# Optimization experiments

Hardware: AMD Instinct MI355X
Metric: run time of the kernel (lower is better)

## Reference

```python
import jax, jax.numpy as jnp
import numpy as np

B, S, D, NH, NKV, HD, FF = 2, 2048, 2048, 16, 8, 128, 8192
EPS = 1e-6
ROPE_THETA = 10000.0


def rmsnorm(x, w):
    return x * jax.lax.rsqrt(jnp.mean(x * x, axis=-1, keepdims=True) + EPS) * w


def rotate_half(x):
    h = x.shape[-1] // 2
    return jnp.concatenate([-x[..., h:], x[..., :h]], axis=-1)


def setup_inputs() -> dict:
    key = jax.random.key(0)
    ks = jax.random.split(key, 32)
    sc = 0.02
    inp = {}
    inp['x'] = jax.random.normal(ks[0], (B, S, D), dtype=jnp.float32)
    pos = jnp.arange(S, dtype=jnp.float32)
    inv = 1.0 / (ROPE_THETA ** (jnp.arange(0, HD, 2, dtype=jnp.float32) / HD))
    fr = jnp.outer(pos, inv)
    emb = jnp.concatenate([fr, fr], axis=-1)  # [S, HD]
    inp['cos'] = jnp.broadcast_to(jnp.cos(emb)[None], (B, S, HD)).astype(jnp.float32)
    inp['sin'] = jnp.broadcast_to(jnp.sin(emb)[None], (B, S, HD)).astype(jnp.float32)
    inp['vision_token_mask'] = jax.random.randint(ks[1], (B, S), 0, 2) > 0
    inp['attn_norm_w'] = jnp.ones((D,), jnp.float32)
    inp['ffn_norm_w'] = jnp.ones((D,), jnp.float32)
    shapes = {
        'wq': (D, NH * HD), 'wk': (D, NKV * HD), 'wv': (D, NKV * HD), 'wo': (NH * HD, D),
        'mm_wq': (D, NH * HD), 'mm_wk': (D, NKV * HD), 'mm_wv': (D, NKV * HD), 'mm_wo': (NH * HD, D),
        'gate_w': (D, FF), 'up_w': (D, FF), 'down_w': (FF, D),
        'mm_gate_w': (D, FF), 'mm_up_w': (D, FF), 'mm_down_w': (FF, D),
    }
    for i, (name, shp) in enumerate(shapes.items()):
        inp[name] = jax.random.normal(ks[2 + i], shp, dtype=jnp.float32) * sc
    for name in ['q_norm_w', 'k_norm_w', 'mm_q_norm_w', 'mm_k_norm_w']:
        inp[name] = jnp.ones((HD,), jnp.float32)
    return inp


def gpt_block(x, cos, sin, mask, attn_norm_w, ffn_norm_w,
              wq, wk, wv, wo, mm_wq, mm_wk, mm_wv, mm_wo,
              q_norm_w, k_norm_w, mm_q_norm_w, mm_k_norm_w,
              gate_w, up_w, down_w, mm_gate_w, mm_up_w, mm_down_w):
    m2 = mask[..., None]            # [B,S,1]
    m4 = mask[:, :, None, None]     # [B,S,1,1]
    h = rmsnorm(x, attn_norm_w)
    # dual-path QKV: text tokens use plain weights, vision tokens use mm_* weights
    q_t = rmsnorm((h @ wq).reshape(B, S, NH, HD), q_norm_w)
    q_v = rmsnorm((h @ mm_wq).reshape(B, S, NH, HD), mm_q_norm_w)
    q = jnp.where(m4, q_v, q_t)
    k_t = rmsnorm((h @ wk).reshape(B, S, NKV, HD), k_norm_w)
    k_v = rmsnorm((h @ mm_wk).reshape(B, S, NKV, HD), mm_k_norm_w)
    k = jnp.where(m4, k_v, k_t)
    v = jnp.where(m2, h @ mm_wv, h @ wv).reshape(B, S, NKV, HD)
    # RoPE (unsqueeze over head dim)
    cu = cos[:, :, None, :]
    su = sin[:, :, None, :]
    q = q * cu + rotate_half(q) * su
    k = k * cu + rotate_half(k) * su
    # GQA repeat + causal attention
    rep = NH // NKV
    k_r = jnp.repeat(k, rep, axis=2)
    v_r = jnp.repeat(v, rep, axis=2)
    scale = 1.0 / jnp.sqrt(jnp.float32(HD))
    scores = jnp.einsum('bqhd,bkhd->bhqk', q, k_r) * scale
    causal = jnp.tril(jnp.ones((S, S), bool))
    scores = jnp.where(causal, scores, jnp.float32(-1e30))
    p = jax.nn.softmax(scores, axis=-1)
    attn = jnp.einsum('bhqk,bkhd->bqhd', p, v_r).reshape(B, S, NH * HD)
    attn_out = jnp.where(m2, attn @ mm_wo, attn @ wo)
    h2 = x + attn_out
    # dual-path SwiGLU FFN
    g = rmsnorm(h2, ffn_norm_w)
    ff_t = (jax.nn.silu(g @ gate_w) * (g @ up_w)) @ down_w
    ff_v = (jax.nn.silu(g @ mm_gate_w) * (g @ mm_up_w)) @ mm_down_w
    return h2 + jnp.where(m2, ff_v, ff_t)


def reference(x, cos, sin, vision_token_mask, attn_norm_w, ffn_norm_w,
              wq, wk, wv, wo, mm_wq, mm_wk, mm_wv, mm_wo,
              q_norm_w, k_norm_w, mm_q_norm_w, mm_k_norm_w,
              gate_w, up_w, down_w, mm_gate_w, mm_up_w, mm_down_w):
    return gpt_block(x, cos, sin, vision_token_mask, attn_norm_w, ffn_norm_w,
                     wq, wk, wv, wo, mm_wq, mm_wk, mm_wv, mm_wo,
                     q_norm_w, k_norm_w, mm_q_norm_w, mm_k_norm_w,
                     gate_w, up_w, down_w, mm_gate_w, mm_up_w, mm_down_w)
```

## Files before the change

kernel.cpp:

```cpp
#include <hip/hip_runtime.h>

typedef unsigned short u16;
typedef __bf16 bf16x8 __attribute__((ext_vector_type(8)));
typedef float f32x4 __attribute__((ext_vector_type(4)));

__device__ __forceinline__ u16 f2bf(float f) {
    unsigned u = __builtin_bit_cast(unsigned, f);
    u += 0x7fffu + ((u >> 16) & 1u);
    return (u16)(u >> 16);
}
__device__ __forceinline__ float bf2f(u16 v) {
    unsigned u = ((unsigned)v) << 16;
    return __builtin_bit_cast(float, u);
}
__device__ __forceinline__ void glds16(const void* g, void* l) {
    __builtin_amdgcn_global_load_lds(
        (const __attribute__((address_space(1))) unsigned*)g,
        (__attribute__((address_space(3))) unsigned*)l, 16, 0, 0);
}

__device__ __forceinline__ void xcd_map(int bid, int nloc, int& tm, int& tn)
{
    const int TM = 33;
    const int xcd = bid & 7;
    int l = bid >> 3;
    const int per = nloc << 3;
    const int fullC = TM >> 3;
    const int lFull = fullC * per;
    int c, tn_l, tmIn;
    if (l < lFull) { c = l / per; int r = l - c * per; tn_l = r >> 3; tmIn = r & 7; }
    else { int r = l - lFull; int sc = TM - (fullC << 3); c = fullC; tn_l = r / sc; tmIn = r % sc; }
    tm = (c << 3) + tmIn;
    tn = xcd * nloc + tn_l;
}

__global__ __launch_bounds__(1024) void build_perm(
    const int* __restrict__ mask, int* __restrict__ perm, int* __restrict__ counts)
{
    __shared__ int sc[1024];
    int t = threadIdx.x;
    int m[4], cnt = 0;
#pragma unroll
    for (int j = 0; j < 4; j++) {
        m[j] = mask[t * 4 + j] != 0;
        cnt += (m[j] == 0);
    }
    sc[t] = cnt;
    __syncthreads();
    for (int off = 1; off < 1024; off <<= 1) {
        int v = (t >= off) ? sc[t - off] : 0;
        __syncthreads();
        sc[t] += v;
        __syncthreads();
    }
    int totT = sc[1023];
    int exT = sc[t] - cnt;
    int exV = t * 4 - exT;
    int pT = exT, pV = totT + exV;
#pragma unroll
    for (int j = 0; j < 4; j++) {
        if (m[j] == 0) perm[pT++] = t * 4 + j;
        else           perm[pV++] = t * 4 + j;
    }
    if (t == 0) { counts[0] = totT; counts[1] = 4096 - totT; }
}

__global__ __launch_bounds__(256) void transpose_bf16(
    const float* __restrict__ W, u16* __restrict__ Wt, int Kd, int Nd)
{
    __shared__ float tile[32][33];
    int k0 = blockIdx.x * 32, n0 = blockIdx.y * 32;
    int tx = threadIdx.x, ty = threadIdx.y;
#pragma unroll
    for (int i = 0; i < 32; i += 8)
        tile[ty + i][tx] = W[(long)(k0 + ty + i) * Nd + n0 + tx];
    __syncthreads();
#pragma unroll
    for (int i = 0; i < 32; i += 8)
        Wt[(long)(n0 + ty + i) * Kd + k0 + tx] = f2bf(tile[tx][ty + i]);
}

__global__ __launch_bounds__(256) void rms_x(
    const float* __restrict__ x, const float* __restrict__ w, u16* __restrict__ out)
{
    long row = blockIdx.x;
    int t = threadIdx.x, wave = t >> 6, lane = t & 63;
    const float4* x4 = (const float4*)(x + row * 2048);
    float4 a = x4[2 * t], b = x4[2 * t + 1];
    float ss = a.x*a.x + a.y*a.y + a.z*a.z + a.w*a.w
             + b.x*b.x + b.y*b.y + b.z*b.z + b.w*b.w;
#pragma unroll
    for (int m = 1; m < 64; m <<= 1) ss += __shfl_xor(ss, m);
    __shared__ float red[4];
    if (lane == 0) red[wave] = ss;
    __syncthreads();
    float tot = red[0] + red[1] + red[2] + red[3];
    float inv = rsqrtf(tot * (1.0f / 2048.0f) + 1e-6f);
    const float4* w4 = (const float4*)w;
    float4 wa = w4[2 * t], wb = w4[2 * t + 1];
    u16* op = out + row * 2048 + t * 8;
    op[0] = f2bf(a.x * inv * wa.x); op[1] = f2bf(a.y * inv * wa.y);
    op[2] = f2bf(a.z * inv * wa.z); op[3] = f2bf(a.w * inv * wa.w);
    op[4] = f2bf(b.x * inv * wb.x); op[5] = f2bf(b.y * inv * wb.y);
    op[6] = f2bf(b.z * inv * wb.z); op[7] = f2bf(b.w * inv * wb.w);
}

template <int EPI, bool PG, bool PC>
__global__ __launch_bounds__(512, 2) void gemmk(
    const u16* __restrict__ A, const u16* __restrict__ Bt0, const u16* __restrict__ Bt1,
    void* __restrict__ Cv, const float* __restrict__ resid,
    const int* __restrict__ perm, const int* __restrict__ counts, int N, int K)
{
    extern __shared__ u16 lds[];
    int tm, tn;
    xcd_map(blockIdx.x, N >> 11, tm, tn);
    const int nT = counts[0];
    const int tT = (nT + 127) >> 7, tV = (4096 - nT + 127) >> 7;
    if (tm >= tT + tV) return;
    const bool vis = tm >= tT;
    const u16* Bt = vis ? Bt1 : Bt0;
    const int rowbase = vis ? nT + (tm - tT) * 128 : tm * 128;
    const int rowlim = vis ? 4096 : nT;
    const int tid = threadIdx.x;
    const int wave = tid >> 6, lane = tid & 63;
    const int wrbase = (wave >> 2) * 64, wcbase = (wave & 3) * 64;
    const int lr = lane & 15, lg = lane >> 4;
    const int n0 = tn * 256;
    const int t8 = tid >> 3, sp = tid & 7;
    const char* aSrc[2];
    const char* bSrc[4];
#pragma unroll
    for (int c = 0; c < 2; c++) {
        int r = c * 64 + t8;
        int gr = rowbase + r; gr = gr < 4095 ? gr : 4095;
        long ar = PG ? perm[gr] : gr;
        aSrc[c] = (const char*)A + ar * (long)K * 2 + ((sp ^ (r & 7)) << 4);
    }
#pragma unroll
    for (int c = 0; c < 4; c++) {
        int r = c * 64 + t8;
        bSrc[c] = (const char*)Bt + (long)(n0 + r) * K * 2 + ((sp ^ (r & 7)) << 4);
    }
    auto stage = [&](int kt, int bu) {
        char* ab = (char*)lds + bu * 49152;
        char* bb = ab + 16384;
        long ko = (long)kt * 128;
#pragma unroll
        for (int c = 0; c < 2; c++)
            glds16(aSrc[c] + ko, ab + c * 8192 + tid * 16);
#pragma unroll
        for (int c = 0; c < 4; c++)
            glds16(bSrc[c] + ko, bb + c * 8192 + tid * 16);
    };
    auto ldA = [&](int bu, int mi, int kk) -> bf16x8 {
        const char* ab = (const char*)lds + bu * 49152;
        int row = wrbase + mi * 16 + lr;
        int sl = kk * 4 + lg;
        return *(const bf16x8*)(ab + row * 128 + ((sl ^ (row & 7)) << 4));
    };
    auto ldB = [&](int bu, int ni, int kk) -> bf16x8 {
        const char* bb = (const char*)lds + bu * 49152 + 16384;
        int row = wcbase + ni * 16 + lr;
        int sl = kk * 4 + lg;
        return *(const bf16x8*)(bb + row * 128 + ((sl ^ (row & 7)) << 4));
    };

    f32x4 acc[4][4] = {};
    const int nkt = K >> 6;
    stage(0, 0);
    stage(1, 1);
    for (int kt = 0; kt < nkt; ++kt) {
        const int bu = kt % 3;
        if (kt == nkt - 1) asm volatile("s_waitcnt vmcnt(0)" ::: "memory");
        else               asm volatile("s_waitcnt vmcnt(6)" ::: "memory");
        __builtin_amdgcn_s_barrier();
        if (kt + 2 < nkt) stage(kt + 2, (kt + 2) % 3);
#pragma unroll
        for (int kk = 0; kk < 2; kk++) {
            bf16x8 af[4], bq[4];
#pragma unroll
            for (int i = 0; i < 4; i++) af[i] = ldA(bu, i, kk);
#pragma unroll
            for (int j = 0; j < 4; j++) bq[j] = ldB(bu, j, kk);
            __builtin_amdgcn_s_setprio(1);
#pragma unroll
            for (int i = 0; i < 4; i++)
#pragma unroll
                for (int j = 0; j < 4; j++)
                    acc[i][j] = __builtin_amdgcn_mfma_f32_16x16x32_bf16(
                        af[i], bq[j], acc[i][j], 0, 0, 0);
            __builtin_amdgcn_s_setprio(0);
        }
    }
#pragma unroll
    for (int mi = 0; mi < 4; mi++)
#pragma unroll
        for (int r = 0; r < 4; r++) {
            int gr = rowbase + wrbase + mi * 16 + lg * 4 + r;
            if (gr >= rowlim) continue;
            long crow = PC ? (long)perm[gr] : (long)gr;
#pragma unroll
            for (int ni = 0; ni < 4; ni++) {
                long col = n0 + wcbase + ni * 16 + lr;
                long idx = crow * (long)N + col;
                float v = acc[mi][ni][r];
                if (EPI == 1)      ((u16*)Cv)[idx] = f2bf(v);
                else if (EPI == 2) ((float*)Cv)[idx] = resid[idx] + v;
            }
        }
}

__global__ __launch_bounds__(512, 2) void gemm_gu(
    const u16* __restrict__ A,
    const u16* __restrict__ Bg0, const u16* __restrict__ Bg1,
    const u16* __restrict__ Bu0, const u16* __restrict__ Bu1,
    u16* __restrict__ C,
    const int* __restrict__ perm, const int* __restrict__ counts, int N, int K)
{
    extern __shared__ u16 lds[];
    int tm, tn;
    xcd_map(blockIdx.x, N >> 10, tm, tn);
    const int nT = counts[0];
    const int tT = (nT + 127) >> 7, tV = (4096 - nT + 127) >> 7;
    if (tm >= tT + tV) return;
    const bool vis = tm >= tT;
    const u16* Bg = vis ? Bg1 : Bg0;
    const u16* Bu = vis ? Bu1 : Bu0;
    const int rowbase = vis ? nT + (tm - tT) * 128 : tm * 128;
    const int rowlim = vis ? 4096 : nT;
    const int tid = threadIdx.x;
    const int wave = tid >> 6, lane = tid & 63;
    const int wrbase = (wave >> 2) * 64, wcbase = (wave & 3) * 32;
    const int lr = lane & 15, lg = lane >> 4;
    const int n0 = tn * 128;
    const int t8 = tid >> 3, sp = tid & 7;
    const char *aSrc[2], *gSrc[2], *uSrc[2];
#pragma unroll
    for (int c = 0; c < 2; c++) {
        int r = c * 64 + t8;
        int gr = rowbase + r; gr = gr < 4095 ? gr : 4095;
        long ar = (long)perm[gr];
        aSrc[c] = (const char*)A + ar * (long)K * 2 + ((sp ^ (r & 7)) << 4);
        gSrc[c] = (const char*)Bg + (long)(n0 + r) * K * 2 + ((sp ^ (r & 7)) << 4);
        uSrc[c] = (const char*)Bu + (long)(n0 + r) * K * 2 + ((sp ^ (r & 7)) << 4);
    }
    auto stage = [&](int kt, int bu) {
        char* ab = (char*)lds + bu * 49152;
        long ko = (long)kt * 128;
#pragma unroll
        for (int c = 0; c < 2; c++) {
            glds16(aSrc[c] + ko, ab + c * 8192 + tid * 16);
            glds16(gSrc[c] + ko, ab + 16384 + c * 8192 + tid * 16);
            glds16(uSrc[c] + ko, ab + 32768 + c * 8192 + tid * 16);
        }
    };
    auto ld = [&](int bu, int sub, int row, int kk) -> bf16x8 {
        const char* p = (const char*)lds + bu * 49152 + sub * 16384;
        int sl = kk * 4 + lg;
        return *(const bf16x8*)(p + row * 128 + ((sl ^ (row & 7)) << 4));
    };

    f32x4 accg[4][2] = {}, accu[4][2] = {};
    const int nkt = K >> 6;
    stage(0, 0);
    stage(1, 1);
    for (int kt = 0; kt < nkt; ++kt) {
        const int bu = kt % 3;
        if (kt == nkt - 1) asm volatile("s_waitcnt vmcnt(0)" ::: "memory");
        else               asm volatile("s_waitcnt vmcnt(6)" ::: "memory");
        __builtin_amdgcn_s_barrier();
        if (kt + 2 < nkt) stage(kt + 2, (kt + 2) % 3);
#pragma unroll
        for (int kk = 0; kk < 2; kk++) {
            bf16x8 af[4], bg[2], bv[2];
#pragma unroll
            for (int i = 0; i < 4; i++) af[i] = ld(bu, 0, wrbase + i * 16 + lr, kk);
#pragma unroll
            for (int j = 0; j < 2; j++) {
                bg[j] = ld(bu, 1, wcbase + j * 16 + lr, kk);
                bv[j] = ld(bu, 2, wcbase + j * 16 + lr, kk);
            }
            __builtin_amdgcn_s_setprio(1);
#pragma unroll
            for (int i = 0; i < 4; i++)
#pragma unroll
                for (int j = 0; j < 2; j++) {
                    accg[i][j] = __builtin_amdgcn_mfma_f32_16x16x32_bf16(
                        af[i], bg[j], accg[i][j], 0, 0, 0);
                    accu[i][j] = __builtin_amdgcn_mfma_f32_16x16x32_bf16(
                        af[i], bv[j], accu[i][j], 0, 0, 0);
                }
            __builtin_amdgcn_s_setprio(0);
        }
    }
#pragma unroll
    for (int mi = 0; mi < 4; mi++)
#pragma unroll
        for (int r = 0; r < 4; r++) {
            int gr = rowbase + wrbase + mi * 16 + lg * 4 + r;
            if (gr >= rowlim) continue;
#pragma unroll
            for (int ni = 0; ni < 2; ni++) {
                long col = n0 + wcbase + ni * 16 + lr;
                float g = accg[mi][ni][r], u = accu[mi][ni][r];
                C[(long)gr * N + col] = f2bf(g / (1.0f + __expf(-g)) * u);
            }
        }
}

__global__ __launch_bounds__(256) void qk_fuse(
    const u16* __restrict__ p, const int* __restrict__ mask,
    const float* __restrict__ cs, const float* __restrict__ sn,
    const float* __restrict__ nwt, const float* __restrict__ nwv,
    u16* __restrict__ out, int H, int stride)
{
    int wave = threadIdx.x >> 6, lane = threadIdx.x & 63;
    int gw = blockIdx.x * 4 + wave;
    int tok = gw / H, h = gw % H;
    int b = tok >> 11, s = tok & 2047;
    const u16* src = p + (long)tok * stride + h * 128;
    const float* w = mask[tok] ? nwv : nwt;
    int d = lane * 2;
    float yx = bf2f(src[d]), yy = bf2f(src[d + 1]);
    float ss = yx * yx + yy * yy;
#pragma unroll
    for (int m = 1; m < 64; m <<= 1) ss += __shfl_xor(ss, m);
    float inv = rsqrtf(ss * (1.0f / 128.0f) + 1e-6f);
    float y0 = yx * inv * w[d], y1 = yy * inv * w[d + 1];
    float o0 = __shfl_xor(y0, 32), o1 = __shfl_xor(y1, 32);
    float sgn = (lane < 32) ? -1.0f : 1.0f;
    const float* cp = cs + (long)tok * 128 + d;
    const float* sp = sn + (long)tok * 128 + d;
    float r0 = y0 * cp[0] + sgn * o0 * sp[0];
    float r1 = y1 * cp[1] + sgn * o1 * sp[1];
    u16* op = out + (((long)b * H + h) * 2048 + s) * 128 + d;
    op[0] = f2bf(r0); op[1] = f2bf(r1);
}

__global__ __launch_bounds__(256) void v_fuse(
    const u16* __restrict__ vsrc, u16* __restrict__ outv, int stride)
{
    __shared__ u16 tile[32][33];
    int s0 = blockIdx.x * 32, d0 = blockIdx.y * 32;
    int bkv = blockIdx.z, b = bkv >> 3, kv = bkv & 7;
    int tx = threadIdx.x, ty = threadIdx.y;
#pragma unroll
    for (int i = 0; i < 32; i += 8) {
        long tok = (long)b * 2048 + s0 + ty + i;
        tile[ty + i][tx] = vsrc[tok * stride + kv * 128 + d0 + tx];
    }
    __syncthreads();
#pragma unroll
    for (int i = 0; i < 32; i += 8)
        outv[(((long)b * 8 + kv) * 128 + d0 + ty + i) * 2048 + s0 + tx] =
            tile[tx][ty + i];
}

__global__ __launch_bounds__(256) void attn_fwd(
    const u16* __restrict__ q, const u16* __restrict__ k,
    const u16* __restrict__ v, u16* __restrict__ out)
{
    __shared__ u16 Ks[32 * 128];
    __shared__ u16 Vs[128 * 32];
    __shared__ u16 Ps[4][16][40];
    const int tid = threadIdx.x, wave = tid >> 6, lane = tid & 63;
    const int lr = lane & 15, lg = lane >> 4;
    const int b = blockIdx.z, h = blockIdx.y, q0 = blockIdx.x * 64;
    const int kvh = h >> 1;
    const u16* qp = q + (((long)b * 16 + h) * 2048 + q0 + wave * 16) * 128;
    bf16x8 qf[4];
#pragma unroll
    for (int f = 0; f < 4; f++)
        qf[f] = *(const bf16x8*)(qp + (long)lr * 128 + f * 32 + lg * 8);
    const char* kbase = (const char*)(k + ((long)b * 8 + kvh) * 2048 * 128);
    const char* vbase = (const char*)(v + ((long)b * 8 + kvh) * 128 * 2048);
    f32x4 o[8] = {};
    float lsum[4] = {};
    const float sc2 = 0.08838834764831845f * 1.44269504088896f;
    const float MB = 16.5f;
    const int ntiles = (q0 + 64) >> 5;
    for (int t = 0; t < ntiles; ++t) {
        int kv0 = t * 32;
        __syncthreads();
#pragma unroll
        for (int j = 0; j < 2; j++) {
            int L = (j * 4 + wave) * 1024 + lane * 16;
            {
                int row = L >> 8, cb = L & 255;
                glds16(kbase + (long)(kv0 + row) * 256 + (cb ^ ((row & 7) << 4)),
                       (char*)Ks + (j * 4 + wave) * 1024);
            }
            {
                int row = L >> 6, cb = L & 63;
                glds16(vbase + (long)row * 4096 + kv0 * 2 + (cb ^ ((row & 3) << 4)),
                       (char*)Vs + (j * 4 + wave) * 1024);
            }
        }
        __syncthreads();
        f32x4 s[2] = {};
#pragma unroll
        for (int sub = 0; sub < 2; ++sub)
#pragma unroll
            for (int f = 0; f < 4; ++f) {
                int row = sub * 16 + lr;
                int cb = (f * 64 + lg * 16) ^ ((row & 7) << 4);
                bf16x8 kf = *(const bf16x8*)((const char*)Ks + row * 256 + cb);
                s[sub] = __builtin_amdgcn_mfma_f32_16x16x32_bf16(qf[f], kf, s[sub], 0, 0, 0);
            }
#pragma unroll
        for (int r = 0; r < 4; r++) {
            int rowg = q0 + wave * 16 + lg * 4 + r;
            float s0 = s[0][r] * sc2 - MB; if (kv0 + lr > rowg)      s0 = -1e30f;
            float s1 = s[1][r] * sc2 - MB; if (kv0 + 16 + lr > rowg) s1 = -1e30f;
            float p0 = exp2f(s0), p1 = exp2f(s1);
            lsum[r] += p0 + p1;
            int prow = lg * 4 + r;
            Ps[wave][prow][lr] = f2bf(p0);
            Ps[wave][prow][16 + lr] = f2bf(p1);
        }
        bf16x8 pf = *(const bf16x8*)&Ps[wave][lr][lg * 8];
#pragma unroll
        for (int ni = 0; ni < 8; ni++) {
            int row = ni * 16 + lr;
            int cb = (lg * 16) ^ ((row & 3) << 4);
            bf16x8 vf = *(const bf16x8*)((const char*)Vs + row * 64 + cb);
            o[ni] = __builtin_amdgcn_mfma_f32_16x16x32_bf16(pf, vf, o[ni], 0, 0, 0);
        }
    }
#pragma unroll
    for (int r = 0; r < 4; r++)
#pragma unroll
        for (int mm = 1; mm < 16; mm <<= 1) lsum[r] += __shfl_xor(lsum[r], mm);
#pragma unroll
    for (int ni = 0; ni < 8; ni++)
#pragma unroll
        for (int r = 0; r < 4; r++) {
            long row = (long)b * 2048 + q0 + wave * 16 + lg * 4 + r;
            out[row * 2048 + h * 128 + ni * 16 + lr] = f2bf(o[ni][r] / lsum[r]);
        }
}

extern "C" void kernel_launch(void* const* d_in, const int* in_sizes, int n_in,
                              void* d_out, int out_size, void* d_ws, size_t ws_size,
                              hipStream_t stream)
{
    const float* x    = (const float*)d_in[0];
    const float* cosp = (const float*)d_in[1];
    const float* sinp = (const float*)d_in[2];
    const int*   mask = (const int*)d_in[3];
    const float* anw  = (const float*)d_in[4];
    const float* fnw  = (const float*)d_in[5];
    const float* wq   = (const float*)d_in[6];
    const float* wk   = (const float*)d_in[7];
    const float* wv   = (const float*)d_in[8];
    const float* wo   = (const float*)d_in[9];
    const float* mwq  = (const float*)d_in[10];
    const float* mwk  = (const float*)d_in[11];
    const float* mwv  = (const float*)d_in[12];
    const float* mwo  = (const float*)d_in[13];
    const float* gw   = (const float*)d_in[14];
    const float* uw   = (const float*)d_in[15];
    const float* dw   = (const float*)d_in[16];
    const float* mgw  = (const float*)d_in[17];
    const float* muw  = (const float*)d_in[18];
    const float* mdw  = (const float*)d_in[19];
    const float* qnw  = (const float*)d_in[20];
    const float* knw  = (const float*)d_in[21];
    const float* mqnw = (const float*)d_in[22];
    const float* mknw = (const float*)d_in[23];

    char* base = (char*)d_ws;
    u16* wA0   = (u16*)(base);
    u16* wA1   = (u16*)(base + (32u << 20));
    u16* wB0   = (u16*)(base + (64u << 20));
    u16* wB1   = (u16*)(base + (96u << 20));
    u16* hbf   = (u16*)(base + (64u << 20));
    u16* qkv   = (u16*)(base + (80u << 20));
    u16* qb    = (u16*)(base + (112u << 20));
    u16* kb    = (u16*)(base + (128u << 20));
    u16* vb    = (u16*)(base + (136u << 20));
    u16* attnb = (u16*)(base + (144u << 20));
    u16* e1    = (u16*)(base + (128u << 20));
    float* h2  = (float*)(base + (192u << 20));
    u16* gbf   = (u16*)(base + (224u << 20));
    int* perm  = (int*)(base + (240u << 20));
    int* cnts  = perm + 4096;

    hipFuncSetAttribute((const void*)&gemmk<1, true, true>,
                        hipFuncAttributeMaxDynamicSharedMemorySize, 147456);
    hipFuncSetAttribute((const void*)&gemmk<2, true, true>,
                        hipFuncAttributeMaxDynamicSharedMemorySize, 147456);
    hipFuncSetAttribute((const void*)&gemmk<2, false, true>,
                        hipFuncAttributeMaxDynamicSharedMemorySize, 147456);
    hipFuncSetAttribute((const void*)&gemm_gu,
                        hipFuncAttributeMaxDynamicSharedMemorySize, 147456);

    dim3 tb(32, 8);
    auto TR = [&](const float* w, u16* dst, int K, int N) {
        transpose_bf16<<<dim3(K / 32, N / 32), tb, 0, stream>>>(w, dst, K, N);
    };

    build_perm<<<1, 1024, 0, stream>>>(mask, perm, cnts);
    rms_x<<<4096, 256, 0, stream>>>(x, anw, hbf);

    TR(wq, wA0, 2048, 2048);
    TR(wk, wA0 + (long)2048 * 2048, 2048, 1024);
    TR(wv, wA0 + (long)3072 * 2048, 2048, 1024);
    TR(mwq, wA1, 2048, 2048);
    TR(mwk, wA1 + (long)2048 * 2048, 2048, 1024);
    TR(mwv, wA1 + (long)3072 * 2048, 2048, 1024);
    gemmk<1, true, true><<<528, 512, 147456, stream>>>(
        hbf, wA0, wA1, (void*)qkv, nullptr, perm, cnts, 4096, 2048);

    qk_fuse<<<16384, 256, 0, stream>>>(qkv, mask, cosp, sinp, qnw, mqnw, qb, 16, 4096);
    qk_fuse<<<8192, 256, 0, stream>>>(qkv + 2048, mask, cosp, sinp, knw, mknw, kb, 8, 4096);
    v_fuse<<<dim3(64, 4, 16), tb, 0, stream>>>(qkv + 3072, vb, 4096);

    attn_fwd<<<dim3(32, 16, 2), 256, 0, stream>>>(qb, kb, vb, attnb);

    TR(wo, wA0, 2048, 2048); TR(mwo, wA1, 2048, 2048);
    gemmk<2, true, true><<<264, 512, 147456, stream>>>(
        attnb, wA0, wA1, (void*)h2, x, perm, cnts, 2048, 2048);

    rms_x<<<4096, 256, 0, stream>>>(h2, fnw, gbf);

    TR(gw, wA0, 2048, 8192); TR(mgw, wA1, 2048, 8192);
    TR(uw, wB0, 2048, 8192); TR(muw, wB1, 2048, 8192);
    gemm_gu<<<2112, 512, 147456, stream>>>(
        gbf, wA0, wA1, wB0, wB1, e1, perm, cnts, 8192, 2048);
    TR(dw, wA0, 8192, 2048); TR(mdw, wA1, 8192, 2048);
    gemmk<2, false, true><<<264, 512, 147456, stream>>>(
        e1, wA0, wA1, (void*)d_out, h2, perm, cnts, 2048, 8192);
}
```

Baseline: 1.155 ms.

## Interleave global-to-LDS prefetch with MFMA sub-steps using extra barriers

```diff
diff --git a/kernel.cpp b/kernel.cpp
--- a/kernel.cpp
+++ b/kernel.cpp
@@ -141,13 +141,16 @@
         int r = c * 64 + t8;
         bSrc[c] = (const char*)Bt + (long)(n0 + r) * K * 2 + ((sp ^ (r & 7)) << 4);
     }
-    auto stage = [&](int kt, int bu) {
+    auto stageA = [&](int kt, int bu) {
         char* ab = (char*)lds + bu * 49152;
-        char* bb = ab + 16384;
         long ko = (long)kt * 128;
 #pragma unroll
         for (int c = 0; c < 2; c++)
             glds16(aSrc[c] + ko, ab + c * 8192 + tid * 16);
+    };
+    auto stageB = [&](int kt, int bu) {
+        char* bb = (char*)lds + bu * 49152 + 16384;
+        long ko = (long)kt * 128;
 #pragma unroll
         for (int c = 0; c < 4; c++)
             glds16(bSrc[c] + ko, bb + c * 8192 + tid * 16);
@@ -167,14 +170,15 @@
 
     f32x4 acc[4][4] = {};
     const int nkt = K >> 6;
-    stage(0, 0);
-    stage(1, 1);
+    stageA(0, 0); stageB(0, 0);
+    stageA(1, 1); stageB(1, 1);
     for (int kt = 0; kt < nkt; ++kt) {
         const int bu = kt % 3;
         if (kt == nkt - 1) asm volatile("s_waitcnt vmcnt(0)" ::: "memory");
         else               asm volatile("s_waitcnt vmcnt(6)" ::: "memory");
         __builtin_amdgcn_s_barrier();
-        if (kt + 2 < nkt) stage(kt + 2, (kt + 2) % 3);
+        const bool pre = (kt + 2 < nkt);
+        const int nb = (kt + 2) % 3;
 #pragma unroll
         for (int kk = 0; kk < 2; kk++) {
             bf16x8 af[4], bq[4];
@@ -182,6 +186,9 @@
             for (int i = 0; i < 4; i++) af[i] = ldA(bu, i, kk);
 #pragma unroll
             for (int j = 0; j < 4; j++) bq[j] = ldB(bu, j, kk);
+            if (pre) { if (kk == 0) stageA(kt + 2, nb); else stageB(kt + 2, nb); }
+            __builtin_amdgcn_s_barrier();
+            asm volatile("s_waitcnt lgkmcnt(0)" ::: "memory");
             __builtin_amdgcn_s_setprio(1);
 #pragma unroll
             for (int i = 0; i < 4; i++)
@@ -190,6 +197,7 @@
                     acc[i][j] = __builtin_amdgcn_mfma_f32_16x16x32_bf16(
                         af[i], bq[j], acc[i][j], 0, 0, 0);
             __builtin_amdgcn_s_setprio(0);
+            if (kk == 0) __builtin_amdgcn_s_barrier();
         }
     }
 #pragma unroll
@@ -244,15 +252,12 @@
         gSrc[c] = (const char*)Bg + (long)(n0 + r) * K * 2 + ((sp ^ (r & 7)) << 4);
         uSrc[c] = (const char*)Bu + (long)(n0 + r) * K * 2 + ((sp ^ (r & 7)) << 4);
     }
-    auto stage = [&](int kt, int bu) {
+    auto stageH = [&](int kt, int bu, int c) {
         char* ab = (char*)lds + bu * 49152;
         long ko = (long)kt * 128;
-#pragma unroll
-        for (int c = 0; c < 2; c++) {
-            glds16(aSrc[c] + ko, ab + c * 8192 + tid * 16);
-            glds16(gSrc[c] + ko, ab + 16384 + c * 8192 + tid * 16);
-            glds16(uSrc[c] + ko, ab + 32768 + c * 8192 + tid * 16);
-        }
+        glds16(aSrc[c] + ko, ab + c * 8192 + tid * 16);
+        glds16(gSrc[c] + ko, ab + 16384 + c * 8192 + tid * 16);
+        glds16(uSrc[c] + ko, ab + 32768 + c * 8192 + tid * 16);
     };
     auto ld = [&](int bu, int sub, int row, int kk) -> bf16x8 {
         const char* p = (const char*)lds + bu * 49152 + sub * 16384;
@@ -262,14 +267,15 @@
 
     f32x4 accg[4][2] = {}, accu[4][2] = {};
     const int nkt = K >> 6;
-    stage(0, 0);
-    stage(1, 1);
+    stageH(0, 0, 0); stageH(0, 0, 1);
+    stageH(1, 1, 0); stageH(1, 1, 1);
     for (int kt = 0; kt < nkt; ++kt) {
         const int bu = kt % 3;
         if (kt == nkt - 1) asm volatile("s_waitcnt vmcnt(0)" ::: "memory");
         else               asm volatile("s_waitcnt vmcnt(6)" ::: "memory");
         __builtin_amdgcn_s_barrier();
-        if (kt + 2 < nkt) stage(kt + 2, (kt + 2) % 3);
+        const bool pre = (kt + 2 < nkt);
+        const int nb = (kt + 2) % 3;
 #pragma unroll
         for (int kk = 0; kk < 2; kk++) {
             bf16x8 af[4], bg[2], bv[2];
@@ -280,6 +286,9 @@
                 bg[j] = ld(bu, 1, wcbase + j * 16 + lr, kk);
                 bv[j] = ld(bu, 2, wcbase + j * 16 + lr, kk);
             }
+            if (pre) stageH(kt + 2, nb, kk);
+            __builtin_amdgcn_s_barrier();
+            asm volatile("s_waitcnt lgkmcnt(0)" ::: "memory");
             __builtin_amdgcn_s_setprio(1);
 #pragma unroll
             for (int i = 0; i < 4; i++)
@@ -291,6 +300,7 @@
                         af[i], bv[j], accu[i][j], 0, 0, 0);
                 }
             __builtin_amdgcn_s_setprio(0);
+            if (kk == 0) __builtin_amdgcn_s_barrier();
         }
     }
 #pragma unroll
```

Result: no change. 1.164 ms (+0.7%).

## Use 256-row M tiles with BK=32 for QKV and gate/up GEMMs

Applied to the files above, without the earlier changes.

```diff
diff --git a/kernel.cpp b/kernel.cpp
--- a/kernel.cpp
+++ b/kernel.cpp
@@ -19,9 +19,8 @@
         (__attribute__((address_space(3))) unsigned*)l, 16, 0, 0);
 }
 
-__device__ __forceinline__ void xcd_map(int bid, int nloc, int& tm, int& tn)
-{
-    const int TM = 33;
+__device__ __forceinline__ void xcd_map(int bid, int nloc, int TM, int& tm, int& tn)
+{
     const int xcd = bid & 7;
     int l = bid >> 3;
     const int per = nloc << 3;
@@ -106,6 +105,200 @@
 }
 
 template <int EPI, bool PG, bool PC>
+__global__ __launch_bounds__(512, 2) void gemm2(
+    const u16* __restrict__ A, const u16* __restrict__ Bt0, const u16* __restrict__ Bt1,
+    void* __restrict__ Cv,
+    const int* __restrict__ perm, const int* __restrict__ counts, int N, int K, int TM)
+{
+    extern __shared__ u16 lds[];
+    int tm, tn;
+    xcd_map(blockIdx.x, N >> 11, TM, tm, tn);
+    const int nT = counts[0];
+    const int tT = (nT + 255) >> 8, tV = (4096 - nT + 255) >> 8;
+    if (tm >= tT + tV) return;
+    const bool vis = tm >= tT;
+    const u16* Bt = vis ? Bt1 : Bt0;
+    const int rowbase = vis ? nT + (tm - tT) * 256 : tm * 256;
+    const int rowlim = vis ? 4096 : nT;
+    const int tid = threadIdx.x;
+    const int wave = tid >> 6, lane = tid & 63;
+    const int wrbase = (wave >> 2) * 128, wcbase = (wave & 3) * 64;
+    const int lr = lane & 15, lg = lane >> 4;
+    const int n0 = tn * 256;
+    const int t4 = tid >> 2, sp = tid & 3;
+    const char* aSrc[2];
+    const char* bSrc[2];
+#pragma unroll
+    for (int c = 0; c < 2; c++) {
+        int r = c * 128 + t4;
+        int gr = rowbase + r; gr = gr < 4095 ? gr : 4095;
+        long ar = PG ? perm[gr] : gr;
+        aSrc[c] = (const char*)A + ar * (long)K * 2 + ((sp ^ (r & 3)) << 4);
+        bSrc[c] = (const char*)Bt + (long)(n0 + r) * K * 2 + ((sp ^ (r & 3)) << 4);
+    }
+    auto stage = [&](int kt, int bu) {
+        char* ab = (char*)lds + bu * 32768;
+        long ko = (long)kt * 64;
+#pragma unroll
+        for (int c = 0; c < 2; c++)
+            glds16(aSrc[c] + ko, ab + c * 8192 + tid * 16);
+#pragma unroll
+        for (int c = 0; c < 2; c++)
+            glds16(bSrc[c] + ko, ab + 16384 + c * 8192 + tid * 16);
+    };
+    auto ldA = [&](int bu, int mi) -> bf16x8 {
+        const char* ab = (const char*)lds + bu * 32768;
+        int row = wrbase + mi * 16 + lr;
+        return *(const bf16x8*)(ab + row * 64 + ((lg ^ (row & 3)) << 4));
+    };
+    auto ldB = [&](int bu, int ni) -> bf16x8 {
+        const char* bb = (const char*)lds + bu * 32768 + 16384;
+        int row = wcbase + ni * 16 + lr;
+        return *(const bf16x8*)(bb + row * 64 + ((lg ^ (row & 3)) << 4));
+    };
+
+    f32x4 acc[8][4] = {};
+    const int nkt = K >> 5;
+    stage(0, 0);
+    stage(1, 1);
+    for (int kt = 0; kt < nkt; ++kt) {
+        const int bu = kt % 3;
+        if (kt == nkt - 1) asm volatile("s_waitcnt vmcnt(0)" ::: "memory");
+        else               asm volatile("s_waitcnt vmcnt(4)" ::: "memory");
+        __builtin_amdgcn_s_barrier();
+        if (kt + 2 < nkt) stage(kt + 2, (kt + 2) % 3);
+        bf16x8 af[8], bq[4];
+#pragma unroll
+        for (int i = 0; i < 8; i++) af[i] = ldA(bu, i);
+#pragma unroll
+        for (int j = 0; j < 4; j++) bq[j] = ldB(bu, j);
+        __builtin_amdgcn_s_setprio(1);
+#pragma unroll
+        for (int i = 0; i < 8; i++)
+#pragma unroll
+            for (int j = 0; j < 4; j++)
+                acc[i][j] = __builtin_amdgcn_mfma_f32_16x16x32_bf16(
+                    af[i], bq[j], acc[i][j], 0, 0, 0);
+        __builtin_amdgcn_s_setprio(0);
+    }
+#pragma unroll
+    for (int mi = 0; mi < 8; mi++)
+#pragma unroll
+        for (int r = 0; r < 4; r++) {
+            int gr = rowbase + wrbase + mi * 16 + lg * 4 + r;
+            if (gr >= rowlim) continue;
+            long crow = PC ? (long)perm[gr] : (long)gr;
+#pragma unroll
+            for (int ni = 0; ni < 4; ni++) {
+                long col = n0 + wcbase + ni * 16 + lr;
+                ((u16*)Cv)[crow * (long)N + col] = f2bf(acc[mi][ni][r]);
+            }
+        }
+}
+
+__global__ __launch_bounds__(512, 2) void gemm_gu(
+    const u16* __restrict__ A,
+    const u16* __restrict__ Bg0, const u16* __restrict__ Bg1,
+    const u16* __restrict__ Bu0, const u16* __restrict__ Bu1,
+    u16* __restrict__ C,
+    const int* __restrict__ perm, const int* __restrict__ counts, int N, int K, int TM)
+{
+    extern __shared__ u16 lds[];
+    int tm, tn;
+    xcd_map(blockIdx.x, N >> 10, TM, tm, tn);
+    const int nT = counts[0];
+    const int tT = (nT + 255) >> 8, tV = (4096 - nT + 255) >> 8;
+    if (tm >= tT + tV) return;
+    const bool vis = tm >= tT;
+    const u16* Bg = vis ? Bg1 : Bg0;
+    const u16* Bu = vis ? Bu1 : Bu0;
+    const int rowbase = vis ? nT + (tm - tT) * 256 : tm * 256;
+    const int rowlim = vis ? 4096 : nT;
+    const int tid = threadIdx.x;
+    const int wave = tid >> 6, lane = tid & 63;
+    const int wrbase = (wave >> 2) * 128, wcbase = (wave & 3) * 32;
+    const int lr = lane & 15, lg = lane >> 4;
+    const int n0 = tn * 128;
+    const int t4 = tid >> 2, sp = tid & 3;
+    const char *aSrc[2], *gSrc, *uSrc;
+#pragma unroll
+    for (int c = 0; c < 2; c++) {
+        int r = c * 128 + t4;
+        int gr = rowbase + r; gr = gr < 4095 ? gr : 4095;
+        long ar = (long)perm[gr];
+        aSrc[c] = (const char*)A + ar * (long)K * 2 + ((sp ^ (r & 3)) << 4);
+    }
+    {
+        int r = t4;
+        gSrc = (const char*)Bg + (long)(n0 + r) * K * 2 + ((sp ^ (r & 3)) << 4);
+        uSrc = (const char*)Bu + (long)(n0 + r) * K * 2 + ((sp ^ (r & 3)) << 4);
+    }
+    auto stage = [&](int kt, int bu) {
+        char* ab = (char*)lds + bu * 32768;
+        long ko = (long)kt * 64;
+#pragma unroll
+        for (int c = 0; c < 2; c++)
+            glds16(aSrc[c] + ko, ab + c * 8192 + tid * 16);
+        glds16(gSrc + ko, ab + 16384 + tid * 16);
+        glds16(uSrc + ko, ab + 24576 + tid * 16);
+    };
+    auto ldA = [&](int bu, int mi) -> bf16x8 {
+        const char* ab = (const char*)lds + bu * 32768;
+        int row = wrbase + mi * 16 + lr;
+        return *(const bf16x8*)(ab + row * 64 + ((lg ^ (row & 3)) << 4));
+    };
+    auto ldGU = [&](int bu, int sub, int ni) -> bf16x8 {
+        const char* p = (const char*)lds + bu * 32768 + 16384 + sub * 8192;
+        int row = wcbase + ni * 16 + lr;
+        return *(const bf16x8*)(p + row * 64 + ((lg ^ (row & 3)) << 4));
+    };
+
+    f32x4 accg[8][2] = {}, accu[8][2] = {};
+    const int nkt = K >> 5;
+    stage(0, 0);
+    stage(1, 1);
+    for (int kt = 0; kt < nkt; ++kt) {
+        const int bu = kt % 3;
+        if (kt == nkt - 1) asm volatile("s_waitcnt vmcnt(0)" ::: "memory");
+        else               asm volatile("s_waitcnt vmcnt(4)" ::: "memory");
+        __builtin_amdgcn_s_barrier();
+        if (kt + 2 < nkt) stage(kt + 2, (kt + 2) % 3);
+        bf16x8 af[8], bg[2], bv[2];
+#pragma unroll
+        for (int i = 0; i < 8; i++) af[i] = ldA(bu, i);
+#pragma unroll
+        for (int j = 0; j < 2; j++) {
+            bg[j] = ldGU(bu, 0, j);
+            bv[j] = ldGU(bu, 1, j);
+        }
+        __builtin_amdgcn_s_setprio(1);
+#pragma unroll
+        for (int i = 0; i < 8; i++)
+#pragma unroll
+            for (int j = 0; j < 2; j++) {
+                accg[i][j] = __builtin_amdgcn_mfma_f32_16x16x32_bf16(
+                    af[i], bg[j], accg[i][j], 0, 0, 0);
+                accu[i][j] = __builtin_amdgcn_mfma_f32_16x16x32_bf16(
+                    af[i], bv[j], accu[i][j], 0, 0, 0);
+            }
+        __builtin_amdgcn_s_setprio(0);
+    }
+#pragma unroll
+    for (int mi = 0; mi < 8; mi++)
+#pragma unroll
+        for (int r = 0; r < 4; r++) {
+            int gr = rowbase + wrbase + mi * 16 + lg * 4 + r;
+            if (gr >= rowlim) continue;
+#pragma unroll
+            for (int ni = 0; ni < 2; ni++) {
+                long col = n0 + wcbase + ni * 16 + lr;
+                float g = accg[mi][ni][r], u = accu[mi][ni][r];
+                C[(long)gr * N + col] = f2bf(g / (1.0f + __expf(-g)) * u);
+            }
+        }
+}
+
+template <int EPI, bool PG, bool PC>
 __global__ __launch_bounds__(512, 2) void gemmk(
     const u16* __restrict__ A, const u16* __restrict__ Bt0, const u16* __restrict__ Bt1,
     void* __restrict__ Cv, const float* __restrict__ resid,
@@ -113,7 +306,7 @@
 {
     extern __shared__ u16 lds[];
     int tm, tn;
-    xcd_map(blockIdx.x, N >> 11, tm, tn);
+    xcd_map(blockIdx.x, N >> 11, 33, tm, tn);
     const int nT = counts[0];
     const int tT = (nT + 127) >> 7, tV = (4096 - nT + 127) >> 7;
     if (tm >= tT + tV) return;
@@ -206,104 +399,6 @@
                 float v = acc[mi][ni][r];
                 if (EPI == 1)      ((u16*)Cv)[idx] = f2bf(v);
                 else if (EPI == 2) ((float*)Cv)[idx] = resid[idx] + v;
-            }
-        }
-}
-
-__global__ __launch_bounds__(512, 2) void gemm_gu(
-    const u16* __restrict__ A,
-    const u16* __restrict__ Bg0, const u16* __restrict__ Bg1,
-    const u16* __restrict__ Bu0, const u16* __restrict__ Bu1,
-    u16* __restrict__ C,
-    const int* __restrict__ perm, const int* __restrict__ counts, int N, int K)
-{
-    extern __shared__ u16 lds[];
-    int tm, tn;
-    xcd_map(blockIdx.x, N >> 10, tm, tn);
-    const int nT = counts[0];
-    const int tT = (nT + 127) >> 7, tV = (4096 - nT + 127) >> 7;
-    if (tm >= tT + tV) return;
-    const bool vis = tm >= tT;
-    const u16* Bg = vis ? Bg1 : Bg0;
-    const u16* Bu = vis ? Bu1 : Bu0;
-    const int rowbase = vis ? nT + (tm - tT) * 128 : tm * 128;
-    const int rowlim = vis ? 4096 : nT;
-    const int tid = threadIdx.x;
-    const int wave = tid >> 6, lane = tid & 63;
-    const int wrbase = (wave >> 2) * 64, wcbase = (wave & 3) * 32;
-    const int lr = lane & 15, lg = lane >> 4;
-    const int n0 = tn * 128;
-    const int t8 = tid >> 3, sp = tid & 7;
-    const char *aSrc[2], *gSrc[2], *uSrc[2];
-#pragma unroll
-    for (int c = 0; c < 2; c++) {
-        int r = c * 64 + t8;
-        int gr = rowbase + r; gr = gr < 4095 ? gr : 4095;
-        long ar = (long)perm[gr];
-        aSrc[c] = (const char*)A + ar * (long)K * 2 + ((sp ^ (r & 7)) << 4);
-        gSrc[c] = (const char*)Bg + (long)(n0 + r) * K * 2 + ((sp ^ (r & 7)) << 4);
-        uSrc[c] = (const char*)Bu + (long)(n0 + r) * K * 2 + ((sp ^ (r & 7)) << 4);
-    }
-    auto stage = [&](int kt, int bu) {
-        char* ab = (char*)lds + bu * 49152;
-        long ko = (long)kt * 128;
-#pragma unroll
-        for (int c = 0; c < 2; c++) {
-            glds16(aSrc[c] + ko, ab + c * 8192 + tid * 16);
-            glds16(gSrc[c] + ko, ab + 16384 + c * 8192 + tid * 16);
-            glds16(uSrc[c] + ko, ab + 32768 + c * 8192 + tid * 16);
-        }
-    };
-    auto ld = [&](int bu, int sub, int row, int kk) -> bf16x8 {
-        const char* p = (const char*)lds + bu * 49152 + sub * 16384;
-        int sl = kk * 4 + lg;
-        return *(const bf16x8*)(p + row * 128 + ((sl ^ (row & 7)) << 4));
-    };
-
-    f32x4 accg[4][2] = {}, accu[4][2] = {};
-    const int nkt = K >> 6;
-    stage(0, 0);
-    stage(1, 1);
-    for (int kt = 0; kt < nkt; ++kt) {
-        const int bu = kt % 3;
-        if (kt == nkt - 1) asm volatile("s_waitcnt vmcnt(0)" ::: "memory");
-        else               asm volatile("s_waitcnt vmcnt(6)" ::: "memory");
-        __builtin_amdgcn_s_barrier();
-        if (kt + 2 < nkt) stage(kt + 2, (kt + 2) % 3);
-#pragma unroll
-        for (int kk = 0; kk < 2; kk++) {
-            bf16x8 af[4], bg[2], bv[2];
-#pragma unroll
-            for (int i = 0; i < 4; i++) af[i] = ld(bu, 0, wrbase + i * 16 + lr, kk);
-#pragma unroll
-            for (int j = 0; j < 2; j++) {
-                bg[j] = ld(bu, 1, wcbase + j * 16 + lr, kk);
-                bv[j] = ld(bu, 2, wcbase + j * 16 + lr, kk);
-            }
-            __builtin_amdgcn_s_setprio(1);
-#pragma unroll
-            for (int i = 0; i < 4; i++)
-#pragma unroll
-                for (int j = 0; j < 2; j++) {
-                    accg[i][j] = __builtin_amdgcn_mfma_f32_16x16x32_bf16(
-                        af[i], bg[j], accg[i][j], 0, 0, 0);
-                    accu[i][j] = __builtin_amdgcn_mfma_f32_16x16x32_bf16(
-                        af[i], bv[j], accu[i][j], 0, 0, 0);
-                }
-            __builtin_amdgcn_s_setprio(0);
-        }
-    }
-#pragma unroll
-    for (int mi = 0; mi < 4; mi++)
-#pragma unroll
-        for (int r = 0; r < 4; r++) {
-            int gr = rowbase + wrbase + mi * 16 + lg * 4 + r;
-            if (gr >= rowlim) continue;
-#pragma unroll
-            for (int ni = 0; ni < 2; ni++) {
-                long col = n0 + wcbase + ni * 16 + lr;
-                float g = accg[mi][ni][r], u = accu[mi][ni][r];
-                C[(long)gr * N + col] = f2bf(g / (1.0f + __expf(-g)) * u);
             }
         }
 }
@@ -486,13 +581,13 @@
     int* perm  = (int*)(base + (240u << 20));
     int* cnts  = perm + 4096;
 
-    hipFuncSetAttribute((const void*)&gemmk<1, true, true>,
-                        hipFuncAttributeMaxDynamicSharedMemorySize, 147456);
+    hipFuncSetAttribute((const void*)&gemm2<1, true, true>,
+                        hipFuncAttributeMaxDynamicSharedMemorySize, 98304);
+    hipFuncSetAttribute((const void*)&gemm_gu,
+                        hipFuncAttributeMaxDynamicSharedMemorySize, 98304);
     hipFuncSetAttribute((const void*)&gemmk<2, true, true>,
                         hipFuncAttributeMaxDynamicSharedMemorySize, 147456);
     hipFuncSetAttribute((const void*)&gemmk<2, false, true>,
-                        hipFuncAttributeMaxDynamicSharedMemorySize, 147456);
-    hipFuncSetAttribute((const void*)&gemm_gu,
                         hipFuncAttributeMaxDynamicSharedMemorySize, 147456);
 
     dim3 tb(32, 8);
@@ -509,8 +604,8 @@
     TR(mwq, wA1, 2048, 2048);
     TR(mwk, wA1 + (long)2048 * 2048, 2048, 1024);
     TR(mwv, wA1 + (long)3072 * 2048, 2048, 1024);
-    gemmk<1, true, true><<<528, 512, 147456, stream>>>(
-        hbf, wA0, wA1, (void*)qkv, nullptr, perm, cnts, 4096, 2048);
+    gemm2<1, true, true><<<272, 512, 98304, stream>>>(
+        hbf, wA0, wA1, (void*)qkv, perm, cnts, 4096, 2048, 17);
 
     qk_fuse<<<16384, 256, 0, stream>>>(qkv, mask, cosp, sinp, qnw, mqnw, qb, 16, 4096);
     qk_fuse<<<8192, 256, 0, stream>>>(qkv + 2048, mask, cosp, sinp, knw, mknw, kb, 8, 4096);
@@ -526,8 +621,8 @@
 
     TR(gw, wA0, 2048, 8192); TR(mgw, wA1, 2048, 8192);
     TR(uw, wB0, 2048, 8192); TR(muw, wB1, 2048, 8192);
-    gemm_gu<<<2112, 512, 147456, stream>>>(
-        gbf, wA0, wA1, wB0, wB1, e1, perm, cnts, 8192, 2048);
+    gemm_gu<<<1088, 512, 98304, stream>>>(
+        gbf, wA0, wA1, wB0, wB1, e1, perm, cnts, 8192, 2048, 17);
     TR(dw, wA0, 8192, 2048); TR(mdw, wA1, 8192, 2048);
     gemmk<2, false, true><<<264, 512, 147456, stream>>>(
         e1, wA0, wA1, (void*)d_out, h2, perm, cnts, 2048, 8192);
```

Result: no change. 1.167 ms (+1.1%).

## Add 256x256-tile GEMM kernel and split gate/up into two passes

Applied to the files above, without the earlier changes.

```diff
diff --git a/kernel.cpp b/kernel.cpp
--- a/kernel.cpp
+++ b/kernel.cpp
@@ -19,9 +19,8 @@
         (__attribute__((address_space(3))) unsigned*)l, 16, 0, 0);
 }
 
-__device__ __forceinline__ void xcd_map(int bid, int nloc, int& tm, int& tn)
-{
-    const int TM = 33;
+__device__ __forceinline__ void xcd_map(int bid, int nloc, int TM, int& tm, int& tn)
+{
     const int xcd = bid & 7;
     int l = bid >> 3;
     const int per = nloc << 3;
@@ -106,6 +105,125 @@
 }
 
 template <int EPI, bool PG, bool PC>
+__global__ __launch_bounds__(512, 2) void gemm8(
+    const u16* __restrict__ A, const u16* __restrict__ Bt0, const u16* __restrict__ Bt1,
+    void* __restrict__ Cv,
+    const int* __restrict__ perm, const int* __restrict__ counts, int N, int K)
+{
+    extern __shared__ u16 lds[];
+    int tm, tn;
+    xcd_map(blockIdx.x, N >> 11, 17, tm, tn);
+    const int nT = counts[0];
+    const int tT = (nT + 255) >> 8, tV = (4096 - nT + 255) >> 8;
+    if (tm >= tT + tV) return;
+    const bool vis = tm >= tT;
+    const u16* Bt = vis ? Bt1 : Bt0;
+    const int rowbase = vis ? nT + (tm - tT) * 256 : tm * 256;
+    const int rowlim = vis ? 4096 : nT;
+    const int tid = threadIdx.x;
+    const int wave = tid >> 6, lane = tid & 63;
+    const int wrbase = (wave >> 2) * 128, wcbase = (wave & 3) * 64;
+    const int lr = lane & 15, lg = lane >> 4;
+    const int n0 = tn * 256;
+    const int t4 = tid >> 2, sp = tid & 3;
+    const char* aSrc[2];
+    const char* bSrc[2];
+#pragma unroll
+    for (int g = 0; g < 2; g++) {
+        int r = g * 128 + t4;
+        int gr = rowbase + r; gr = gr < 4095 ? gr : 4095;
+        long ar = PG ? (long)perm[gr] : (long)gr;
+        aSrc[g] = (const char*)A + ar * (long)K * 2 + ((sp ^ ((r >> 1) & 3)) << 4);
+        bSrc[g] = (const char*)Bt + (long)(n0 + r) * K * 2 + ((sp ^ ((r >> 1) & 3)) << 4);
+    }
+    auto stageA = [&](int t) {
+        char* ab = (char*)lds + (t & 3) * 32768;
+        long ko = (long)t * 64;
+#pragma unroll
+        for (int g = 0; g < 2; g++)
+            glds16(aSrc[g] + ko, ab + g * 8192 + tid * 16);
+    };
+    auto stageB = [&](int t) {
+        char* bb = (char*)lds + (t & 3) * 32768 + 16384;
+        long ko = (long)t * 64;
+#pragma unroll
+        for (int g = 0; g < 2; g++)
+            glds16(bSrc[g] + ko, bb + g * 8192 + tid * 16);
+    };
+    auto ldA = [&](int t, int mi) -> bf16x8 {
+        const char* ab = (const char*)lds + (t & 3) * 32768;
+        int row = wrbase + mi * 16 + lr;
+        return *(const bf16x8*)(ab + row * 64 + ((lg ^ ((row >> 1) & 3)) << 4));
+    };
+    auto ldB = [&](int t, int ni) -> bf16x8 {
+        const char* bb = (const char*)lds + (t & 3) * 32768 + 16384;
+        int row = wcbase + ni * 16 + lr;
+        return *(const bf16x8*)(bb + row * 64 + ((lg ^ ((row >> 1) & 3)) << 4));
+    };
+
+    f32x4 acc[8][4] = {};
+    const int nkt = K >> 5;
+    stageA(0); stageB(0); stageA(1);
+    for (int t = 0; t < nkt; ++t) {
+        if (t + 1 < nkt) {
+            stageB(t + 1);
+            asm volatile("s_waitcnt vmcnt(4)" ::: "memory");
+        } else {
+            asm volatile("s_waitcnt vmcnt(0)" ::: "memory");
+        }
+        __builtin_amdgcn_s_barrier();
+        bf16x8 bq[4], af[4];
+#pragma unroll
+        for (int j = 0; j < 4; j++) bq[j] = ldB(t, j);
+#pragma unroll
+        for (int i = 0; i < 4; i++) af[i] = ldA(t, i);
+        asm volatile("s_waitcnt lgkmcnt(0)" ::: "memory");
+        __builtin_amdgcn_s_setprio(1);
+#pragma unroll
+        for (int i = 0; i < 4; i++)
+#pragma unroll
+            for (int j = 0; j < 4; j++)
+                acc[i][j] = __builtin_amdgcn_mfma_f32_16x16x32_bf16(
+                    af[i], bq[j], acc[i][j], 0, 0, 0);
+        __builtin_amdgcn_s_setprio(0);
+        __builtin_amdgcn_s_barrier();
+#pragma unroll
+        for (int i = 0; i < 4; i++) af[i] = ldA(t, 4 + i);
+        if (t + 2 < nkt) stageA(t + 2);
+        __builtin_amdgcn_s_barrier();
+        asm volatile("s_waitcnt lgkmcnt(0)" ::: "memory");
+        __builtin_amdgcn_s_setprio(1);
+#pragma unroll
+        for (int i = 0; i < 4; i++)
+#pragma unroll
+            for (int j = 0; j < 4; j++)
+                acc[4 + i][j] = __builtin_amdgcn_mfma_f32_16x16x32_bf16(
+                    af[i], bq[j], acc[4 + i][j], 0, 0, 0);
+        __builtin_amdgcn_s_setprio(0);
+        __builtin_amdgcn_s_barrier();
+    }
+#pragma unroll
+    for (int mi = 0; mi < 8; mi++)
+#pragma unroll
+        for (int r = 0; r < 4; r++) {
+            int gr = rowbase + wrbase + mi * 16 + lg * 4 + r;
+            if (gr >= rowlim) continue;
+            long crow = PC ? (long)perm[gr] : (long)gr;
+#pragma unroll
+            for (int ni = 0; ni < 4; ni++) {
+                long col = n0 + wcbase + ni * 16 + lr;
+                long idx = crow * (long)N + col;
+                float v = acc[mi][ni][r];
+                if (EPI == 1) ((u16*)Cv)[idx] = f2bf(v);
+                else if (EPI == 3) {
+                    float g = bf2f(((u16*)Cv)[idx]);
+                    ((u16*)Cv)[idx] = f2bf(g / (1.0f + __expf(-g)) * v);
+                }
+            }
+        }
+}
+
+template <int EPI, bool PG, bool PC>
 __global__ __launch_bounds__(512, 2) void gemmk(
     const u16* __restrict__ A, const u16* __restrict__ Bt0, const u16* __restrict__ Bt1,
     void* __restrict__ Cv, const float* __restrict__ resid,
@@ -113,7 +231,7 @@
 {
     extern __shared__ u16 lds[];
     int tm, tn;
-    xcd_map(blockIdx.x, N >> 11, tm, tn);
+    xcd_map(blockIdx.x, N >> 11, 33, tm, tn);
     const int nT = counts[0];
     const int tT = (nT + 127) >> 7, tV = (4096 - nT + 127) >> 7;
     if (tm >= tT + tV) return;
@@ -210,104 +328,6 @@
         }
 }
 
-__global__ __launch_bounds__(512, 2) void gemm_gu(
-    const u16* __restrict__ A,
-    const u16* __restrict__ Bg0, const u16* __restrict__ Bg1,
-    const u16* __restrict__ Bu0, const u16* __restrict__ Bu1,
-    u16* __restrict__ C,
-    const int* __restrict__ perm, const int* __restrict__ counts, int N, int K)
-{
-    extern __shared__ u16 lds[];
-    int tm, tn;
-    xcd_map(blockIdx.x, N >> 10, tm, tn);
-    const int nT = counts[0];
-    const int tT = (nT + 127) >> 7, tV = (4096 - nT + 127) >> 7;
-    if (tm >= tT + tV) return;
-    const bool vis = tm >= tT;
-    const u16* Bg = vis ? Bg1 : Bg0;
-    const u16* Bu = vis ? Bu1 : Bu0;
-    const int rowbase = vis ? nT + (tm - tT) * 128 : tm * 128;
-    const int rowlim = vis ? 4096 : nT;
-    const int tid = threadIdx.x;
-    const int wave = tid >> 6, lane = tid & 63;
-    const int wrbase = (wave >> 2) * 64, wcbase = (wave & 3) * 32;
-    const int lr = lane & 15, lg = lane >> 4;
-    const int n0 = tn * 128;
-    const int t8 = tid >> 3, sp = tid & 7;
-    const char *aSrc[2], *gSrc[2], *uSrc[2];
-#pragma unroll
-    for (int c = 0; c < 2; c++) {
-        int r = c * 64 + t8;
-        int gr = rowbase + r; gr = gr < 4095 ? gr : 4095;
-        long ar = (long)perm[gr];
-        aSrc[c] = (const char*)A + ar * (long)K * 2 + ((sp ^ (r & 7)) << 4);
-        gSrc[c] = (const char*)Bg + (long)(n0 + r) * K * 2 + ((sp ^ (r & 7)) << 4);
-        uSrc[c] = (const char*)Bu + (long)(n0 + r) * K * 2 + ((sp ^ (r & 7)) << 4);
-    }
-    auto stage = [&](int kt, int bu) {
-        char* ab = (char*)lds + bu * 49152;
-        long ko = (long)kt * 128;
-#pragma unroll
-        for (int c = 0; c < 2; c++) {
-            glds16(aSrc[c] + ko, ab + c * 8192 + tid * 16);
-            glds16(gSrc[c] + ko, ab + 16384 + c * 8192 + tid * 16);
-            glds16(uSrc[c] + ko, ab + 32768 + c * 8192 + tid * 16);
-        }
-    };
-    auto ld = [&](int bu, int sub, int row, int kk) -> bf16x8 {
-        const char* p = (const char*)lds + bu * 49152 + sub * 16384;
-        int sl = kk * 4 + lg;
-        return *(const bf16x8*)(p + row * 128 + ((sl ^ (row & 7)) << 4));
-    };
-
-    f32x4 accg[4][2] = {}, accu[4][2] = {};
-    const int nkt = K >> 6;
-    stage(0, 0);
-    stage(1, 1);
-    for (int kt = 0; kt < nkt; ++kt) {
-        const int bu = kt % 3;
-        if (kt == nkt - 1) asm volatile("s_waitcnt vmcnt(0)" ::: "memory");
-        else               asm volatile("s_waitcnt vmcnt(6)" ::: "memory");
-        __builtin_amdgcn_s_barrier();
-        if (kt + 2 < nkt) stage(kt + 2, (kt + 2) % 3);
-#pragma unroll
-        for (int kk = 0; kk < 2; kk++) {
-            bf16x8 af[4], bg[2], bv[2];
-#pragma unroll
-            for (int i = 0; i < 4; i++) af[i] = ld(bu, 0, wrbase + i * 16 + lr, kk);
-#pragma unroll
-            for (int j = 0; j < 2; j++) {
-                bg[j] = ld(bu, 1, wcbase + j * 16 + lr, kk);
-                bv[j] = ld(bu, 2, wcbase + j * 16 + lr, kk);
-            }
-            __builtin_amdgcn_s_setprio(1);
-#pragma unroll
-            for (int i = 0; i < 4; i++)
-#pragma unroll
-                for (int j = 0; j < 2; j++) {
-                    accg[i][j] = __builtin_amdgcn_mfma_f32_16x16x32_bf16(
-                        af[i], bg[j], accg[i][j], 0, 0, 0);
-                    accu[i][j] = __builtin_amdgcn_mfma_f32_16x16x32_bf16(
-                        af[i], bv[j], accu[i][j], 0, 0, 0);
-                }
-            __builtin_amdgcn_s_setprio(0);
-        }
-    }
-#pragma unroll
-    for (int mi = 0; mi < 4; mi++)
-#pragma unroll
-        for (int r = 0; r < 4; r++) {
-            int gr = rowbase + wrbase + mi * 16 + lg * 4 + r;
-            if (gr >= rowlim) continue;
-#pragma unroll
-            for (int ni = 0; ni < 2; ni++) {
-                long col = n0 + wcbase + ni * 16 + lr;
-                float g = accg[mi][ni][r], u = accu[mi][ni][r];
-                C[(long)gr * N + col] = f2bf(g / (1.0f + __expf(-g)) * u);
-            }
-        }
-}
-
 __global__ __launch_bounds__(256) void qk_fuse(
     const u16* __restrict__ p, const int* __restrict__ mask,
     const float* __restrict__ cs, const float* __restrict__ sn,
@@ -330,9 +350,9 @@
     float o0 = __shfl_xor(y0, 32), o1 = __shfl_xor(y1, 32);
     float sgn = (lane < 32) ? -1.0f : 1.0f;
     const float* cp = cs + (long)tok * 128 + d;
-    const float* sp = sn + (long)tok * 128 + d;
-    float r0 = y0 * cp[0] + sgn * o0 * sp[0];
-    float r1 = y1 * cp[1] + sgn * o1 * sp[1];
+    const float* spn = sn + (long)tok * 128 + d;
+    float r0 = y0 * cp[0] + sgn * o0 * spn[0];
+    float r1 = y1 * cp[1] + sgn * o1 * spn[1];
     u16* op = out + (((long)b * H + h) * 2048 + s) * 128 + d;
     op[0] = f2bf(r0); op[1] = f2bf(r1);
 }
@@ -486,13 +506,15 @@
     int* perm  = (int*)(base + (240u << 20));
     int* cnts  = perm + 4096;
 
-    hipFuncSetAttribute((const void*)&gemmk<1, true, true>,
-                        hipFuncAttributeMaxDynamicSharedMemorySize, 147456);
+    hipFuncSetAttribute((const void*)&gemm8<1, true, true>,
+                        hipFuncAttributeMaxDynamicSharedMemorySize, 131072);
+    hipFuncSetAttribute((const void*)&gemm8<1, true, false>,
+                        hipFuncAttributeMaxDynamicSharedMemorySize, 131072);
+    hipFuncSetAttribute((const void*)&gemm8<3, true, false>,
+                        hipFuncAttributeMaxDynamicSharedMemorySize, 131072);
     hipFuncSetAttribute((const void*)&gemmk<2, true, true>,
                         hipFuncAttributeMaxDynamicSharedMemorySize, 147456);
     hipFuncSetAttribute((const void*)&gemmk<2, false, true>,
-                        hipFuncAttributeMaxDynamicSharedMemorySize, 147456);
-    hipFuncSetAttribute((const void*)&gemm_gu,
                         hipFuncAttributeMaxDynamicSharedMemorySize, 147456);
 
     dim3 tb(32, 8);
@@ -509,8 +531,8 @@
     TR(mwq, wA1, 2048, 2048);
     TR(mwk, wA1 + (long)2048 * 2048, 2048, 1024);
     TR(mwv, wA1 + (long)3072 * 2048, 2048, 1024);
-    gemmk<1, true, true><<<528, 512, 147456, stream>>>(
-        hbf, wA0, wA1, (void*)qkv, nullptr, perm, cnts, 4096, 2048);
+    gemm8<1, true, true><<<272, 512, 131072, stream>>>(
+        hbf, wA0, wA1, (void*)qkv, perm, cnts, 4096, 2048);
 
     qk_fuse<<<16384, 256, 0, stream>>>(qkv, mask, cosp, sinp, qnw, mqnw, qb, 16, 4096);
     qk_fuse<<<8192, 256, 0, stream>>>(qkv + 2048, mask, cosp, sinp, knw, mknw, kb, 8, 4096);
@@ -526,8 +548,10 @@
 
     TR(gw, wA0, 2048, 8192); TR(mgw, wA1, 2048, 8192);
     TR(uw, wB0, 2048, 8192); TR(muw, wB1, 2048, 8192);
-    gemm_gu<<<2112, 512, 147456, stream>>>(
-        gbf, wA0, wA1, wB0, wB1, e1, perm, cnts, 8192, 2048);
+    gemm8<1, true, false><<<544, 512, 131072, stream>>>(
+        gbf, wA0, wA1, (void*)e1, perm, cnts, 8192, 2048);
+    gemm8<3, true, false><<<544, 512, 131072, stream>>>(
+        gbf, wB0, wB1, (void*)e1, perm, cnts, 8192, 2048);
     TR(dw, wA0, 8192, 2048); TR(mdw, wA1, 8192, 2048);
     gemmk<2, false, true><<<264, 512, 147456, stream>>>(
         e1, wA0, wA1, (void*)d_out, h2, perm, cnts, 2048, 8192);
```

Measured after the change: 1.227 ms. 1.06x slower.
